# Kernel tuning notes

Hardware: AMD Instinct MI355X
Metric: run time of the kernel (lower is better)

Reference implementation:

```python
import jax, jax.numpy as jnp
import numpy as np
from jax import lax

K = 7          # attention window (attn_conv_props.kernel_size)
PAD = K // 2   # 'same' zero padding


def conv1x1(x, W, b):
    # x: (B, Cin, H, W), W: (Cout, Cin), b: (Cout,)
    return jnp.einsum('bchw,oc->bohw', x, W) + b[None, :, None, None]


def unfold(x, k=K):
    # torch Unfold with 'same' zero padding: (B, C, H, W) -> (B, C, k*k, H, W)
    # lax patches are channel-major over the C*k*k feature dim, matching torch.
    B, C, H, W = x.shape
    p = lax.conv_general_dilated_patches(
        x, filter_shape=(k, k), window_strides=(1, 1),
        padding=((PAD, PAD), (PAD, PAD)))
    return p.reshape(B, C, k * k, H, W)


def setup_inputs() -> dict:
    key = jax.random.key(0)
    ks = jax.random.split(key, 8)
    B, Cin, H, W = 2, 128, 64, 64
    heads, dk, dv, Cout = 8, 32, 32, 128
    s_in = 0.02
    return {
        'x':  jax.random.normal(ks[0], (B, Cin, H, W), jnp.float32),
        'Wk': jax.random.normal(ks[1], (heads * dk, Cin), jnp.float32) * s_in,
        'bk': jnp.zeros((heads * dk,), jnp.float32),
        'Wq': jax.random.normal(ks[2], (heads * dk, Cin), jnp.float32) * s_in,
        'bq': jnp.zeros((heads * dk,), jnp.float32),
        'Wv': jax.random.normal(ks[3], (heads * dv, Cin), jnp.float32) * s_in,
        'bv': jnp.zeros((heads * dv,), jnp.float32),
        'Wo': jax.random.normal(ks[4], (Cout, heads * dv), jnp.float32) * s_in,
        'bo': jnp.zeros((Cout,), jnp.float32),
    }


def reference(x, Wk, bk, Wq, bq, Wv, bv, Wo, bo):
    B, Cin, H, W = x.shape
    heads, dk = 8, 32
    dv = 32

    k = conv1x1(x, Wk, bk)   # (B, heads*dk, H, W)
    q = conv1x1(x, Wq, bq)   # (B, heads*dk, H, W)
    v = conv1x1(x, Wv, bv)   # (B, heads*dv, H, W)

    k_unf = unfold(k).reshape(B, heads, dk, K * K, H, W)  # (B,h,dk,A,H,W)
    v_unf = unfold(v).reshape(B, heads, dv, K * K, H, W)  # (B,h,dv,A,H,W)
    q_h = q.reshape(B, heads, dk, H, W)                   # (B,h,dk,H,W)

    scale = jnp.sqrt(jnp.asarray(dk, jnp.float32))
    # per-pixel window logits: (B, h, H, W, A)
    logits = jnp.einsum('bhdxy,bhdaxy->bhxya', q_h, k_unf) / scale
    score = jax.nn.softmax(logits, axis=-1)
    # attend over window: (B, h, dv, H, W)
    attn = jnp.einsum('bhxya,bhdaxy->bhdxy', score, v_unf)
    attn = attn.reshape(B, heads * dv, H, W)

    return conv1x1(attn, Wo, bo)  # (B, Cout, H, W)
```

## Files before the change

kernel.cpp:

```cpp
#include <hip/hip_runtime.h>
#include <hip/hip_bf16.h>
#include <math.h>

constexpr int HW = 4096;

using bf8   = __attribute__((ext_vector_type(8))) short;
using f32x4 = __attribute__((ext_vector_type(4))) float;

constexpr float SCALE = 0.17677669529663687f;


__global__ __launch_bounds__(256) void qkv_fused(
    const float* __restrict__ x,
    const float* __restrict__ Wk, const float* __restrict__ Wq,
    const float* __restrict__ Wv, const float* __restrict__ Wo,
    const float* __restrict__ bk, const float* __restrict__ bq,
    const float* __restrict__ bv,
    unsigned short* __restrict__ Qb, unsigned short* __restrict__ Kc,
    unsigned short* __restrict__ Vc, __hip_bfloat16* __restrict__ Wob)
{
    int bx = blockIdx.x, y = blockIdx.y;
    int t  = threadIdx.x;

    if (bx >= 128) {
        int bid2 = (bx - 128) * 12 + y;
        int base = bid2 * 256 + t;
        const int STR = 48 * 256;
        for (int i = base; i < 120832; i += STR) {
            int plane = i / 236;
            int c8    = i - plane * 236;
            int byteoff;
            if (c8 < 108) {
                int r6  = c8 / 18;
                int o8  = c8 - r6 * 18;
                int row = r6 < 3 ? r6 : 64 + r6;
                byteoff = row * 160 + o8 * 8;
            } else {
                int s   = c8 - 108;
                int row = 3 + (s >> 1);
                byteoff = row * 160 + ((s & 1) ? 136 : 0);
            }
            *(uint2*)((char*)Vc + (size_t)plane * 11200 + byteoff) = make_uint2(0u, 0u);
        }
        for (int i = base; i < 51456; i += STR) {
            int b   = i >= 25728;
            int r   = i - 25728 * b;
            int pxi = r >> 5;
            int sub = r & 31;
            int yy, xx;
            if (pxi < 420) {
                int r70 = pxi / 70;
                yy = r70 < 3 ? r70 : 64 + r70;
                xx = pxi - r70 * 70;
            } else {
                int q = pxi - 420;
                yy = q / 6 + 3;
                int c6 = q - (yy - 3) * 6;
                xx = c6 < 3 ? c6 : 64 + c6;
            }
            *(uint4*)&Kc[((size_t)b * 4900 + yy * 70 + xx) * 256 + sub * 8] =
                make_uint4(0u, 0u, 0u, 0u);
        }
        for (int i = base; i < 32768; i += STR)
            Wob[i] = __float2bfloat16(Wo[i]);
        return;
    }

    __shared__ __align__(16) unsigned short Xl[8192];
    __shared__ __align__(16) unsigned short Wl[8192];

    int b   = bx >> 6;
    int px0 = bx * 64;
    int hw0 = px0 & 4095;
    const float* Wm   = y < 4 ? Wk : (y < 8 ? Wq : Wv);
    const float* bias = y < 4 ? bk : (y < 8 ? bq : bv);
    int ocl = (y & 3) * 64;

    {
        int px = t >> 2;
        int q  = t & 3;
        int wv = px >> 4, mm = px & 15;
        const float* xp = x + ((size_t)b * 128 + q * 32) * HW + hw0 + px;
        int dbase = (wv * 4 + q) * 512 + mm * 8;
        #pragma unroll
        for (int kq = 0; kq < 4; ++kq) {
            union { __hip_bfloat16 hh[8]; uint4 u; } pk;
            #pragma unroll
            for (int j = 0; j < 8; ++j)
                pk.hh[j] = __float2bfloat16(xp[(size_t)(kq * 8 + j) * HW]);
            *(uint4*)&Xl[dbase + kq * 128] = pk.u;
        }
    }
    {
        int oc = t >> 2;
        int q  = t & 3;
        int of = oc >> 4, mm = oc & 15;
        const float* wp = Wm + (size_t)(ocl + oc) * 128 + q * 32;
        int dbase = (of * 4 + q) * 512 + mm * 8;
        #pragma unroll
        for (int kq = 0; kq < 4; ++kq) {
            float4 a0 = *(const float4*)(wp + kq * 8);
            float4 a1 = *(const float4*)(wp + kq * 8 + 4);
            union { __hip_bfloat16 hh[8]; uint4 u; } pk;
            pk.hh[0] = __float2bfloat16(a0.x); pk.hh[1] = __float2bfloat16(a0.y);
            pk.hh[2] = __float2bfloat16(a0.z); pk.hh[3] = __float2bfloat16(a0.w);
            pk.hh[4] = __float2bfloat16(a1.x); pk.hh[5] = __float2bfloat16(a1.y);
            pk.hh[6] = __float2bfloat16(a1.z); pk.hh[7] = __float2bfloat16(a1.w);
            *(uint4*)&Wl[dbase + kq * 128] = pk.u;
        }
    }
    __syncthreads();

    int w = t >> 6, lane = t & 63;
    int m  = lane & 15;
    int kq = lane >> 4;
    int pxw = px0 + w * 16;

    bf8 aF[4];
    #pragma unroll
    for (int ks = 0; ks < 4; ++ks)
        aF[ks] = *(const bf8*)&Xl[(w * 4 + ks) * 512 + lane * 8];

    f32x4 acc[4] = { {0.f,0.f,0.f,0.f}, {0.f,0.f,0.f,0.f},
                     {0.f,0.f,0.f,0.f}, {0.f,0.f,0.f,0.f} };
    #pragma unroll
    for (int ks = 0; ks < 4; ++ks) {
        #pragma unroll
        for (int of = 0; of < 4; ++of) {
            bf8 bF = *(const bf8*)&Wl[(of * 4 + ks) * 512 + lane * 8];
            acc[of] = __builtin_amdgcn_mfma_f32_16x16x32_bf16(aF[ks], bF, acc[of], 0, 0, 0);
        }
    }

    if (y >= 4 && y < 8) {
        #pragma unroll
        for (int of = 0; of < 4; ++of) {
            float bval = bias[ocl + of * 16 + m];
            #pragma unroll
            for (int r = 0; r < 4; ++r) {
                int px = pxw + kq * 4 + r;
                float v = (acc[of][r] + bval) * SCALE;
                __hip_bfloat16 hv = __float2bfloat16(v);
                unsigned us = *(unsigned short*)&hv;
                unsigned un = __shfl_xor((int)us, 1);
                if (!(m & 1))
                    *(unsigned*)&Qb[(size_t)px * 256 + ocl + of * 16 + m] = us | (un << 16);
            }
        }
    } else if (y < 4) {
        #pragma unroll
        for (int of = 0; of < 4; ++of) {
            float bval = bias[ocl + of * 16 + m];
            #pragma unroll
            for (int r = 0; r < 4; ++r) {
                int px = pxw + kq * 4 + r;
                int bb = px >> 12, hw = px & 4095;
                int yy = hw >> 6, xx = hw & 63;
                __hip_bfloat16 hv = __float2bfloat16(acc[of][r] + bval);
                unsigned us = *(unsigned short*)&hv;
                unsigned un = __shfl_xor((int)us, 1);
                if (!(m & 1))
                    *(unsigned*)&Kc[((size_t)bb * 4900 + (yy + 3) * 70 + xx + 3) * 256
                                    + ocl + of * 16 + m] = us | (un << 16);
            }
        }
    } else {
        #pragma unroll
        for (int of = 0; of < 4; ++of) {
            float bval = bias[ocl + of * 16 + m];
            int ch = ocl + of * 16 + m;
            union { __hip_bfloat16 h[4]; uint2 u; } pk;
            #pragma unroll
            for (int r = 0; r < 4; ++r)
                pk.h[r] = __float2bfloat16(acc[of][r] + bval);
            int px = pxw + kq * 4;
            int bb = px >> 12, hw = px & 4095;
            int yy = hw >> 6, xx = hw & 63;
            *(uint2*)&Vc[((size_t)bb * 256 + ch) * 5600 + (yy + 3) * 80 + xx + 4] = pk.u;
        }
    }
}

__global__ __launch_bounds__(256) void attn_win(
    const unsigned short* __restrict__ Qb, const unsigned short* __restrict__ Kc,
    const unsigned short* __restrict__ Vc, unsigned short* __restrict__ ab)
{
    __shared__ __align__(16) unsigned short P[4 * 16 * 136];

    int id   = blockIdx.x;
    int b    = id >> 9;
    int h    = (id >> 6) & 7;
    int tile = id & 63;
    int ty0  = (tile >> 3) * 8;
    int tx0  = (tile & 7) * 8;

    int t  = threadIdx.x;
    int w  = t >> 6;
    int l  = t & 63;
    int lr = l & 15;
    int g  = l >> 4;

    int apy = 2 * w + (lr >> 3);
    int apx = lr & 7;
    bf8 aQ = *(const bf8*)(Qb +
        ((size_t)b * 4096 + (ty0 + apy) * 64 + tx0 + apx) * 256 + h * 32 + g * 8);

    const unsigned short* kcb = Kc + (size_t)b * (4900 * 256) + h * 32 + g * 8;
    f32x4 acc[8];
    #pragma unroll
    for (int i = 0; i < 8; ++i) {
        int nt = 2 * w + i;
        bf8 bK = *(const bf8*)(kcb + ((size_t)(ty0 + nt) * 70 + tx0 + lr - 1) * 256);
        f32x4 z = {0.f, 0.f, 0.f, 0.f};
        acc[i] = __builtin_amdgcn_mfma_f32_16x16x32_bf16(aQ, bK, z, 0, 0, 0);
    }

    int gy2 = g >> 1;
    int xc  = lr;
    unsigned short* pw = &P[w * 2176];
    float rsum[4] = {0.f, 0.f, 0.f, 0.f};
    #pragma unroll
    for (int i = 0; i < 8; ++i) {
        bool dyok = ((unsigned)(i - gy2)) <= 6u;
        #pragma unroll
        for (int reg = 0; reg < 4; ++reg) {
            int px_ = ((g & 1) << 2) + reg;
            bool ok = dyok && (((unsigned)(xc - px_ - 1)) <= 6u);
            float e = ok ? __expf(acc[i][reg]) : 0.f;
            rsum[reg] += e;
            __hip_bfloat16 hb = __float2bfloat16(e);
            unsigned us = *(unsigned short*)&hb;
            unsigned un = __shfl_xor((int)us, 1);
            if (!(l & 1))
                *(unsigned*)&pw[(g * 4 + reg) * 136 + i * 16 + xc] = us | (un << 16);
        }
    }

    #pragma unroll
    for (int reg = 0; reg < 4; ++reg) {
        float s = rsum[reg];
        s += __shfl_xor(s, 1);
        s += __shfl_xor(s, 2);
        s += __shfl_xor(s, 4);
        s += __shfl_xor(s, 8);
        rsum[reg] = 1.f / s;
    }

    f32x4 pv[2] = { {0.f,0.f,0.f,0.f}, {0.f,0.f,0.f,0.f} };
    #pragma unroll
    for (int s = 0; s < 4; ++s) {
        bf8 aP = *(const bf8*)&pw[lr * 136 + s * 32 + g * 8];
        int yq = 2 * w + 2 * s + (g >> 1);
        int xv = (g & 1) << 3;
        #pragma unroll
        for (int nt2 = 0; nt2 < 2; ++nt2) {
            bf8 bV = *(const bf8*)(Vc +
                ((size_t)b * 256 + h * 32 + nt2 * 16 + lr) * 5600 +
                (ty0 + yq) * 80 + tx0 + xv);
            pv[nt2] = __builtin_amdgcn_mfma_f32_16x16x32_bf16(aP, bV, pv[nt2], 0, 0, 0);
        }
    }

    #pragma unroll
    for (int nt2 = 0; nt2 < 2; ++nt2) {
        #pragma unroll
        for (int reg = 0; reg < 4; ++reg) {
            float ov = pv[nt2][reg] * rsum[reg];
            __hip_bfloat16 hb = __float2bfloat16(ov);
            unsigned us = *(unsigned short*)&hb;
            unsigned un = __shfl_xor((int)us, 1);
            if (!(l & 1)) {
                int q_  = g * 4 + reg;
                int py_ = 2 * w + (q_ >> 3);
                int px_ = q_ & 7;
                *(unsigned*)&ab[((size_t)b * 4096 + (ty0 + py_) * 64 + tx0 + px_) * 256
                                + h * 32 + nt2 * 16 + lr] = us | (un << 16);
            }
        }
    }
}

__global__ __launch_bounds__(256) void proj_mfma(
    const __hip_bfloat16* __restrict__ aT, const __hip_bfloat16* __restrict__ Wob,
    const float* __restrict__ bo, float* __restrict__ out)
{
    __shared__ float OutT[32][68];

    int t = threadIdx.x;
    int w = t >> 6, lane = t & 63;
    int m  = lane & 15;
    int kq = lane >> 4;
    int pw = w & 1, ow = w >> 1;
    int px0 = blockIdx.x * 32 + pw * 16;
    int ocb = blockIdx.y * 64 + ow * 32;

    const short* ar = (const short*)aT + (size_t)(px0 + m) * 256;
    f32x4 acc[2] = { {0.f,0.f,0.f,0.f}, {0.f,0.f,0.f,0.f} };
    #pragma unroll
    for (int ks = 0; ks < 8; ++ks) {
        bf8 aF = *(const bf8*)(ar + ks * 32 + kq * 8);
        #pragma unroll
        for (int of = 0; of < 2; ++of) {
            bf8 bF = *(const bf8*)((const short*)Wob +
                     (size_t)(ocb + of * 16 + m) * 256 + ks * 32 + kq * 8);
            acc[of] = __builtin_amdgcn_mfma_f32_16x16x32_bf16(aF, bF, acc[of], 0, 0, 0);
        }
    }

    #pragma unroll
    for (int of = 0; of < 2; ++of) {
        float bval = bo[ocb + of * 16 + m];
        #pragma unroll
        for (int r = 0; r < 4; ++r)
            OutT[pw * 16 + kq * 4 + r][ow * 32 + of * 16 + m] = acc[of][r] + bval;
    }
    __syncthreads();

    int pxl = t & 31, ocg = t >> 5;
    int gpx = blockIdx.x * 32 + pxl;
    int b   = gpx >> 12, hw = gpx & 4095;
    #pragma unroll
    for (int i = 0; i < 8; ++i) {
        int oc = blockIdx.y * 64 + ocg * 8 + i;
        out[((size_t)b * 128 + oc) * HW + hw] = OutT[pxl][ocg * 8 + i];
    }
}

extern "C" void kernel_launch(void* const* d_in, const int* in_sizes, int n_in,
                              void* d_out, int out_size, void* d_ws, size_t ws_size,
                              hipStream_t stream) {
    const float* x  = (const float*)d_in[0];
    const float* Wk = (const float*)d_in[1];
    const float* bk = (const float*)d_in[2];
    const float* Wq = (const float*)d_in[3];
    const float* bq = (const float*)d_in[4];
    const float* Wv = (const float*)d_in[5];
    const float* bv = (const float*)d_in[6];
    const float* Wo = (const float*)d_in[7];
    const float* bo = (const float*)d_in[8];
    float* out = (float*)d_out;

    char* wsb = (char*)d_ws;
    unsigned short* Qb  = (unsigned short*)wsb;
    unsigned short* Kc  = (unsigned short*)(wsb + (4u << 20));
    unsigned short* Vc  = (unsigned short*)(wsb + (9u << 20));
    __hip_bfloat16* Wob = (__hip_bfloat16*)(wsb + (15u << 20));
    __hip_bfloat16* abT = (__hip_bfloat16*)(wsb + (16u << 20));

    qkv_fused<<<dim3(132, 12), 256, 0, stream>>>(
        x, Wk, Wq, Wv, Wo, bk, bq, bv, Qb, Kc, Vc, Wob);
    attn_win<<<dim3(1024), 256, 0, stream>>>(Qb, Kc, Vc, (unsigned short*)abT);
    proj_mfma<<<dim3(256, 2), 256, 0, stream>>>(abT, Wob, bo, out);
}
```

Before: 45.41 us.

## Fuse windowed attention and output projection into one kernel

Merges the attention kernel and the 1x1 output projection into a single 512-thread kernel. Each block covers a 4x8 pixel tile across all 8 heads, one wave per head, and stages the bf16 attention output in shared memory. After a block barrier, the same block runs the projection MFMAs from shared memory and writes float4 outputs directly. This drops the global round trip of the intermediate attention tensor and one launch, at the cost of fewer blocks (256), a larger block, more LDS, and a barrier.

Measured after the change: 44.61 us. About the same (-1.8%).

```diff
diff --git a/kernel.cpp b/kernel.cpp
--- a/kernel.cpp
+++ b/kernel.cpp
@@ -181,17 +181,18 @@
     }
 }
 
-__global__ __launch_bounds__(256) void attn_win(
+__global__ __launch_bounds__(512) void attn_proj(
     const unsigned short* __restrict__ Qb, const unsigned short* __restrict__ Kc,
-    const unsigned short* __restrict__ Vc, unsigned short* __restrict__ ab)
+    const unsigned short* __restrict__ Vc, const __hip_bfloat16* __restrict__ Wob,
+    const float* __restrict__ bo, float* __restrict__ out)
 {
-    __shared__ __align__(16) unsigned short P[4 * 16 * 136];
+    __shared__ __align__(16) unsigned short P[8 * 2176];
+    __shared__ __align__(16) unsigned short AB[32 * 264];
 
     int id   = blockIdx.x;
-    int b    = id >> 9;
-    int h    = (id >> 6) & 7;
-    int tile = id & 63;
-    int ty0  = (tile >> 3) * 8;
+    int b    = id >> 7;
+    int tile = id & 127;
+    int ty0  = (tile >> 3) * 4;
     int tx0  = (tile & 7) * 8;
 
     int t  = threadIdx.x;
@@ -199,130 +200,111 @@
     int l  = t & 63;
     int lr = l & 15;
     int g  = l >> 4;
-
-    int apy = 2 * w + (lr >> 3);
-    int apx = lr & 7;
-    bf8 aQ = *(const bf8*)(Qb +
-        ((size_t)b * 4096 + (ty0 + apy) * 64 + tx0 + apx) * 256 + h * 32 + g * 8);
-
+    int h  = w;
+
+    unsigned short* pw = &P[w * 2176];
     const unsigned short* kcb = Kc + (size_t)b * (4900 * 256) + h * 32 + g * 8;
-    f32x4 acc[8];
-    #pragma unroll
-    for (int i = 0; i < 8; ++i) {
-        int nt = 2 * w + i;
-        bf8 bK = *(const bf8*)(kcb + ((size_t)(ty0 + nt) * 70 + tx0 + lr - 1) * 256);
-        f32x4 z = {0.f, 0.f, 0.f, 0.f};
-        acc[i] = __builtin_amdgcn_mfma_f32_16x16x32_bf16(aQ, bK, z, 0, 0, 0);
-    }
-
-    int gy2 = g >> 1;
-    int xc  = lr;
-    unsigned short* pw = &P[w * 2176];
-    float rsum[4] = {0.f, 0.f, 0.f, 0.f};
-    #pragma unroll
-    for (int i = 0; i < 8; ++i) {
-        bool dyok = ((unsigned)(i - gy2)) <= 6u;
+
+    #pragma unroll
+    for (int s = 0; s < 2; ++s) {
+        int apy = 2 * s + (lr >> 3);
+        int apx = lr & 7;
+        bf8 aQ = *(const bf8*)(Qb +
+            ((size_t)b * 4096 + (ty0 + apy) * 64 + tx0 + apx) * 256 + h * 32 + g * 8);
+
+        f32x4 acc[8];
+        #pragma unroll
+        for (int i = 0; i < 8; ++i) {
+            bf8 bK = *(const bf8*)(kcb +
+                ((size_t)(ty0 + 2 * s + i) * 70 + tx0 + lr - 1) * 256);
+            f32x4 z = {0.f, 0.f, 0.f, 0.f};
+            acc[i] = __builtin_amdgcn_mfma_f32_16x16x32_bf16(aQ, bK, z, 0, 0, 0);
+        }
+
+        int gy2 = g >> 1;
+        float rsum[4] = {0.f, 0.f, 0.f, 0.f};
+        #pragma unroll
+        for (int i = 0; i < 8; ++i) {
+            bool dyok = ((unsigned)(i - gy2)) <= 6u;
+            #pragma unroll
+            for (int reg = 0; reg < 4; ++reg) {
+                int px_ = ((g & 1) << 2) + reg;
+                bool ok = dyok && (((unsigned)(lr - px_ - 1)) <= 6u);
+                float e = ok ? __expf(acc[i][reg]) : 0.f;
+                rsum[reg] += e;
+                __hip_bfloat16 hb = __float2bfloat16(e);
+                unsigned us = *(unsigned short*)&hb;
+                unsigned un = __shfl_xor((int)us, 1);
+                if (!(l & 1))
+                    *(unsigned*)&pw[(g * 4 + reg) * 136 + i * 16 + lr] = us | (un << 16);
+            }
+        }
         #pragma unroll
         for (int reg = 0; reg < 4; ++reg) {
-            int px_ = ((g & 1) << 2) + reg;
-            bool ok = dyok && (((unsigned)(xc - px_ - 1)) <= 6u);
-            float e = ok ? __expf(acc[i][reg]) : 0.f;
-            rsum[reg] += e;
-            __hip_bfloat16 hb = __float2bfloat16(e);
-            unsigned us = *(unsigned short*)&hb;
-            unsigned un = __shfl_xor((int)us, 1);
-            if (!(l & 1))
-                *(unsigned*)&pw[(g * 4 + reg) * 136 + i * 16 + xc] = us | (un << 16);
-        }
-    }
-
-    #pragma unroll
-    for (int reg = 0; reg < 4; ++reg) {
-        float s = rsum[reg];
-        s += __shfl_xor(s, 1);
-        s += __shfl_xor(s, 2);
-        s += __shfl_xor(s, 4);
-        s += __shfl_xor(s, 8);
-        rsum[reg] = 1.f / s;
-    }
-
-    f32x4 pv[2] = { {0.f,0.f,0.f,0.f}, {0.f,0.f,0.f,0.f} };
-    #pragma unroll
-    for (int s = 0; s < 4; ++s) {
-        bf8 aP = *(const bf8*)&pw[lr * 136 + s * 32 + g * 8];
-        int yq = 2 * w + 2 * s + (g >> 1);
-        int xv = (g & 1) << 3;
+            float sm = rsum[reg];
+            sm += __shfl_xor(sm, 1);
+            sm += __shfl_xor(sm, 2);
+            sm += __shfl_xor(sm, 4);
+            sm += __shfl_xor(sm, 8);
+            rsum[reg] = 1.f / sm;
+        }
+
+        f32x4 pv[2] = { {0.f,0.f,0.f,0.f}, {0.f,0.f,0.f,0.f} };
+        #pragma unroll
+        for (int ks = 0; ks < 4; ++ks) {
+            bf8 aP = *(const bf8*)&pw[lr * 136 + ks * 32 + g * 8];
+            int yq = 2 * s + 2 * ks + (g >> 1);
+            int xv = (g & 1) << 3;
+            #pragma unroll
+            for (int nt2 = 0; nt2 < 2; ++nt2) {
+                bf8 bV = *(const bf8*)(Vc +
+                    ((size_t)b * 256 + h * 32 + nt2 * 16 + lr) * 5600 +
+                    (ty0 + yq) * 80 + tx0 + xv);
+                pv[nt2] = __builtin_amdgcn_mfma_f32_16x16x32_bf16(aP, bV, pv[nt2], 0, 0, 0);
+            }
+        }
+
         #pragma unroll
         for (int nt2 = 0; nt2 < 2; ++nt2) {
-            bf8 bV = *(const bf8*)(Vc +
-                ((size_t)b * 256 + h * 32 + nt2 * 16 + lr) * 5600 +
-                (ty0 + yq) * 80 + tx0 + xv);
-            pv[nt2] = __builtin_amdgcn_mfma_f32_16x16x32_bf16(aP, bV, pv[nt2], 0, 0, 0);
-        }
-    }
-
-    #pragma unroll
-    for (int nt2 = 0; nt2 < 2; ++nt2) {
-        #pragma unroll
-        for (int reg = 0; reg < 4; ++reg) {
-            float ov = pv[nt2][reg] * rsum[reg];
-            __hip_bfloat16 hb = __float2bfloat16(ov);
-            unsigned us = *(unsigned short*)&hb;
-            unsigned un = __shfl_xor((int)us, 1);
-            if (!(l & 1)) {
-                int q_  = g * 4 + reg;
-                int py_ = 2 * w + (q_ >> 3);
-                int px_ = q_ & 7;
-                *(unsigned*)&ab[((size_t)b * 4096 + (ty0 + py_) * 64 + tx0 + px_) * 256
-                                + h * 32 + nt2 * 16 + lr] = us | (un << 16);
-            }
-        }
-    }
-}
-
-__global__ __launch_bounds__(256) void proj_mfma(
-    const __hip_bfloat16* __restrict__ aT, const __hip_bfloat16* __restrict__ Wob,
-    const float* __restrict__ bo, float* __restrict__ out)
-{
-    __shared__ float OutT[32][68];
-
-    int t = threadIdx.x;
-    int w = t >> 6, lane = t & 63;
-    int m  = lane & 15;
-    int kq = lane >> 4;
-    int pw = w & 1, ow = w >> 1;
-    int px0 = blockIdx.x * 32 + pw * 16;
-    int ocb = blockIdx.y * 64 + ow * 32;
-
-    const short* ar = (const short*)aT + (size_t)(px0 + m) * 256;
-    f32x4 acc[2] = { {0.f,0.f,0.f,0.f}, {0.f,0.f,0.f,0.f} };
+            #pragma unroll
+            for (int reg = 0; reg < 4; ++reg) {
+                float ov = pv[nt2][reg] * rsum[reg];
+                __hip_bfloat16 hb = __float2bfloat16(ov);
+                unsigned us = *(unsigned short*)&hb;
+                unsigned un = __shfl_xor((int)us, 1);
+                if (!(l & 1)) {
+                    int rloc = s * 16 + g * 4 + reg;
+                    *(unsigned*)&AB[rloc * 264 + h * 32 + nt2 * 16 + lr] = us | (un << 16);
+                }
+            }
+        }
+    }
+    __syncthreads();
+
+    int sp  = w & 1;
+    int ocq = w >> 1;
+    f32x4 po[2] = { {0.f,0.f,0.f,0.f}, {0.f,0.f,0.f,0.f} };
     #pragma unroll
     for (int ks = 0; ks < 8; ++ks) {
-        bf8 aF = *(const bf8*)(ar + ks * 32 + kq * 8);
+        bf8 aA = *(const bf8*)&AB[(sp * 16 + lr) * 264 + ks * 32 + g * 8];
         #pragma unroll
         for (int of = 0; of < 2; ++of) {
-            bf8 bF = *(const bf8*)((const short*)Wob +
-                     (size_t)(ocb + of * 16 + m) * 256 + ks * 32 + kq * 8);
-            acc[of] = __builtin_amdgcn_mfma_f32_16x16x32_bf16(aF, bF, acc[of], 0, 0, 0);
-        }
-    }
-
+            int oc16 = ocq * 32 + of * 16;
+            bf8 bF = *(const bf8*)((const unsigned short*)Wob +
+                     (size_t)(oc16 + lr) * 256 + ks * 32 + g * 8);
+            po[of] = __builtin_amdgcn_mfma_f32_16x16x32_bf16(aA, bF, po[of], 0, 0, 0);
+        }
+    }
     #pragma unroll
     for (int of = 0; of < 2; ++of) {
-        float bval = bo[ocb + of * 16 + m];
-        #pragma unroll
-        for (int r = 0; r < 4; ++r)
-            OutT[pw * 16 + kq * 4 + r][ow * 32 + of * 16 + m] = acc[of][r] + bval;
-    }
-    __syncthreads();
-
-    int pxl = t & 31, ocg = t >> 5;
-    int gpx = blockIdx.x * 32 + pxl;
-    int b   = gpx >> 12, hw = gpx & 4095;
-    #pragma unroll
-    for (int i = 0; i < 8; ++i) {
-        int oc = blockIdx.y * 64 + ocg * 8 + i;
-        out[((size_t)b * 128 + oc) * HW + hw] = OutT[pxl][ocg * 8 + i];
+        int oc = ocq * 32 + of * 16 + lr;
+        float bval = bo[oc];
+        int pxl = sp * 16 + g * 4;
+        int py  = pxl >> 3;
+        int px_ = pxl & 7;
+        float4 r4 = make_float4(po[of][0] + bval, po[of][1] + bval,
+                                po[of][2] + bval, po[of][3] + bval);
+        *(float4*)&out[((size_t)b * 128 + oc) * 4096 + (ty0 + py) * 64 + tx0 + px_] = r4;
     }
 }
 
@@ -345,10 +327,8 @@
     unsigned short* Kc  = (unsigned short*)(wsb + (4u << 20));
     unsigned short* Vc  = (unsigned short*)(wsb + (9u << 20));
     __hip_bfloat16* Wob = (__hip_bfloat16*)(wsb + (15u << 20));
-    __hip_bfloat16* abT = (__hip_bfloat16*)(wsb + (16u << 20));
 
     qkv_fused<<<dim3(132, 12), 256, 0, stream>>>(
         x, Wk, Wq, Wv, Wo, bk, bq, bv, Qb, Kc, Vc, Wob);
-    attn_win<<<dim3(1024), 256, 0, stream>>>(Qb, Kc, Vc, (unsigned short*)abT);
-    proj_mfma<<<dim3(256, 2), 256, 0, stream>>>(abT, Wob, bo, out);
+    attn_proj<<<dim3(256), 512, 0, stream>>>(Qb, Kc, Vc, Wob, bo, out);
 }
```
